# Performance work log

Measured on AMD Instinct MI355X. Metric: run time of the kernel, lower is better.

Reference implementation:

```python
import jax, jax.numpy as jnp
import numpy as np

D = 1024      # d_model
H = 16        # n_heads
M = 64        # n_memories
DK = D // H   # head dim
EPS = 1e-5    # LayerNorm eps


def setup_inputs() -> dict:
    key = jax.random.key(0)
    ks = jax.random.split(key, 16)
    B, N = 4, 1024
    s = 0.02
    return {
        "queries": jax.random.normal(ks[0], (B, N, D), jnp.float32),
        "keys": jax.random.normal(ks[1], (B, N, D), jnp.float32),
        "values": jax.random.normal(ks[2], (B, N, D), jnp.float32),
        "attention_mask": jax.random.randint(ks[3], (B, 1, 1, N), 0, 2, dtype=jnp.int32),
        "Wq": jax.random.normal(ks[4], (D, D), jnp.float32) * s,
        "bq": jnp.zeros((D,), jnp.float32),
        "Wk": jax.random.normal(ks[5], (D, D), jnp.float32) * s,
        "bk": jnp.zeros((D,), jnp.float32),
        "Wv": jax.random.normal(ks[6], (D, D), jnp.float32) * s,
        "bv": jnp.zeros((D,), jnp.float32),
        "Wo": jax.random.normal(ks[7], (D, D), jnp.float32) * s,
        "bo": jnp.zeros((D,), jnp.float32),
        "m_k": jax.random.normal(ks[8], (1, M, D), jnp.float32) * 0.01,
        "m_v": jax.random.normal(ks[9], (1, M, D), jnp.float32) * 0.01,
        "gamma": jnp.ones((D,), jnp.float32),
        "beta": jnp.zeros((D,), jnp.float32),
    }


def _layer_norm(x, gamma, beta):
    mu = jnp.mean(x, axis=-1, keepdims=True)
    var = jnp.var(x, axis=-1, keepdims=True)
    return (x - mu) * jax.lax.rsqrt(var + EPS) * gamma + beta


def reference(queries, keys, values, attention_mask,
              Wq, bq, Wk, bk, Wv, bv, Wo, bo, m_k, m_v, gamma, beta):
    B, Nq, _ = queries.shape
    Nk = keys.shape[1]
    scale = 1.0 / np.sqrt(DK)

    # projections (torch Linear: x @ W.T + b)
    q = (queries @ Wq.T + bq).reshape(B, Nq, H, DK).transpose(0, 2, 1, 3)  # b h nq d

    # memory-augmented K/V (memory tokens scaled as in the source)
    k_full = jnp.concatenate(
        [keys @ Wk.T + bk, jnp.broadcast_to(m_k * np.sqrt(DK), (B, M, D))], axis=1)
    v_full = jnp.concatenate(
        [values @ Wv.T + bv, jnp.broadcast_to(m_v * np.sqrt(M), (B, M, D))], axis=1)
    k = k_full.reshape(B, Nk + M, H, DK).transpose(0, 2, 1, 3)  # b h nk+m d
    v = v_full.reshape(B, Nk + M, H, DK).transpose(0, 2, 1, 3)  # b h nk+m d

    scores = jnp.einsum('bhqd,bhkd->bhqk', q, k) * scale  # [B,H,Nq,Nk+M]

    # partial masking: only the first Nk (non-memory) columns are maskable
    mask = jnp.concatenate(
        [attention_mask.astype(bool),
         jnp.zeros((B, 1, 1, M), dtype=bool)], axis=-1)
    scores = jnp.where(mask, -jnp.inf, scores)

    p_attn = jax.nn.softmax(scores, axis=-1)  # dropout p=0.0 -> identity
    out = jnp.einsum('bhqk,bhkd->bhqd', p_attn, v)
    out = out.transpose(0, 2, 1, 3).reshape(B, Nq, D)
    out = out @ Wo.T + bo

    # residual + LayerNorm (outer dropout is identity at p=0.0)
    return _layer_norm(queries + out, gamma, beta)
```

## Files before the change

### kernel.cpp

```cpp
#include <hip/hip_runtime.h>


typedef __bf16 bf16;
typedef __bf16 bf16x8 __attribute__((ext_vector_type(8)));
typedef __bf16 bf16x4 __attribute__((ext_vector_type(4)));
typedef float  f32x4  __attribute__((ext_vector_type(4)));

#define NSEQ 1024
#define NKV  1088
#define DMODEL 1024

struct CvtArgs { const float* s[7]; const float* mk; const float* mv; };

__global__ __launch_bounds__(256) void prep(CvtArgs c, bf16* __restrict__ dst,
                                            bf16* __restrict__ Kb,
                                            bf16* __restrict__ Vt)
{
    int blk = blockIdx.x;
    if (blk < 8192) {
        size_t e = ((size_t)blk * 256 + threadIdx.x) * 8;
        const float* s;
        if (e < ((size_t)3 << 22)) {
            s = c.s[e >> 22] + (e & 0x3FFFFF);
        } else {
            size_t wq = e - ((size_t)3 << 22);
            s = c.s[3 + (wq >> 20)] + (wq & 0xFFFFF);
        }
        f32x4 a = *(const f32x4*)s;
        f32x4 b = *(const f32x4*)(s + 4);
        bf16x8 o;
        for (int i = 0; i < 4; i++) { o[i] = (bf16)a[i]; o[4 + i] = (bf16)b[i]; }
        *(bf16x8*)&dst[e] = o;
    } else {
        int i = (blk - 8192) * 256 + threadIdx.x;
        int b = i >> 16, md = i & 65535;
        int m = md >> 10, dcol = md & 1023;
        Kb[(size_t)b * (NKV * DMODEL) + (size_t)(NSEQ + m) * DMODEL + dcol]
            = (bf16)(c.mk[md] * 8.0f);
        Vt[((size_t)b * 1024 + dcol) * NKV + NSEQ + m] = (bf16)(c.mv[md] * 8.0f);
    }
}

typedef __attribute__((address_space(1))) void gas_void;
typedef __attribute__((address_space(3))) void las_void;

__device__ __forceinline__ void gload16(const bf16* g, bf16* l)
{
    __builtin_amdgcn_global_load_lds((gas_void*)g, (las_void*)l, 16, 0, 0);
}

struct GemmArgsB {
    const bf16* A;
    const bf16* W;
    const float* bias;
    bf16* C;
    int osK;
    int vt;
};

__global__ __launch_bounds__(256, 3) void gemm128_lds(GemmArgsB g0, GemmArgsB g1,
                                                      GemmArgsB g2)
{
    const GemmArgsB g = (blockIdx.z == 0) ? g0 : (blockIdx.z == 1) ? g1 : g2;
    __shared__ bf16 As[128][32];
    __shared__ bf16 Bs[128][32];
    const int t = threadIdx.x;
    const int lane = t & 63, w = t >> 6;
    const int qi = lane & 15, qq = lane >> 4;
    const int wrow = (w >> 1) * 64, wcol = (w & 1) * 64;
    const int bm = blockIdx.y * 128, bn = blockIdx.x * 128;

    const int srow = w * 32 + (lane >> 2);
    const int scol = (lane & 3) * 8;
    const bf16* Ag = g.A + (size_t)(bm + srow) * DMODEL + scol;
    const bf16* Wg = g.W + (size_t)(bn + srow) * DMODEL + scol;
    bf16* Al = &As[w * 32][0];
    bf16* Bl = &Bs[w * 32][0];

    f32x4 acc[4][4] = {};

#define STAGE(kt)                                                             \
    do {                                                                      \
        gload16(Ag + (kt),                 Al);                               \
        gload16(Ag + (kt) + 16 * DMODEL,   Al + 16 * 32);                     \
        gload16(Wg + (kt),                 Bl);                               \
        gload16(Wg + (kt) + 16 * DMODEL,   Bl + 16 * 32);                    \
    } while (0)

    STAGE(0);
    for (int kt = 0; kt < DMODEL; kt += 32) {
        __syncthreads();
        bf16x8 a[4], b[4];
        for (int i = 0; i < 4; i++)
            a[i] = *(const bf16x8*)&As[wrow + i * 16 + qi][qq * 8];
        for (int j = 0; j < 4; j++)
            b[j] = *(const bf16x8*)&Bs[wcol + j * 16 + qi][qq * 8];
        __syncthreads();
        if (kt + 32 < DMODEL) STAGE(kt + 32);
        for (int i = 0; i < 4; i++)
            for (int j = 0; j < 4; j++)
                acc[i][j] = __builtin_amdgcn_mfma_f32_16x16x32_bf16(
                    a[i], b[j], acc[i][j], 0, 0, 0);
    }
#undef STAGE

    for (int i = 0; i < 4; i++)
        for (int j = 0; j < 4; j++) {
            int row0 = bm + wrow + i * 16 + qq * 4;
            int col  = bn + wcol + j * 16 + qi;
            float bcol = g.bias[col];
            if (g.vt) {
                bf16x4 v;
                for (int r = 0; r < 4; r++) v[r] = (bf16)(acc[i][j][r] + bcol);
                size_t off = ((size_t)((row0 >> 10) * 16 + (col >> 6)) * 64 + (col & 63))
                           * NKV + (row0 & 1023);
                *(bf16x4*)&g.C[off] = v;
            } else {
                for (int r = 0; r < 4; r++) {
                    int row = row0 + r;
                    size_t off = (size_t)(row >> 10) * g.osK
                               + (size_t)(row & 1023) * DMODEL + col;
                    g.C[off] = (bf16)(acc[i][j][r] + bcol);
                }
            }
        }
}

struct GemmArgs {
    const void* A;
    const float* W;
    const float* bias;
    bf16* C;
    int osK;
    int vt;
};

template<bool ABF>
__global__ __launch_bounds__(256, 2) void gemm128(GemmArgs g0, GemmArgs g1, GemmArgs g2)
{
    const GemmArgs g = (blockIdx.z == 0) ? g0 : (blockIdx.z == 1) ? g1 : g2;
    __shared__ bf16 As[128][44];
    __shared__ bf16 Bs[128][44];
    const int t = threadIdx.x;
    const int lane = t & 63, w = t >> 6;
    const int qi = lane & 15, qq = lane >> 4;
    const int wrow = (w >> 1) * 64, wcol = (w & 1) * 64;
    const int bm = blockIdx.y * 128, bn = blockIdx.x * 128;
    const int sr = t >> 1, sc = (t & 1) * 16;

    f32x4 acc[4][4] = {};

    f32x4 pa[4];
    bf16x8 pab[2];
    f32x4 pw[4];

    const float* Wp = g.W + (size_t)(bn + sr) * DMODEL + sc;
    const float* Af = (const float*)g.A + (size_t)(bm + sr) * DMODEL + sc;
    const bf16*  Ab = (const bf16*)g.A + (size_t)(bm + sr) * DMODEL + sc;

#define LOAD_TILES(kt)                                                        \
    do {                                                                      \
        if (ABF) {                                                            \
            pab[0] = *(const bf16x8*)(Ab + (kt));                             \
            pab[1] = *(const bf16x8*)(Ab + (kt) + 8);                         \
        } else {                                                              \
            pa[0] = *(const f32x4*)(Af + (kt));                               \
            pa[1] = *(const f32x4*)(Af + (kt) + 4);                           \
            pa[2] = *(const f32x4*)(Af + (kt) + 8);                           \
            pa[3] = *(const f32x4*)(Af + (kt) + 12);                          \
        }                                                                     \
        pw[0] = *(const f32x4*)(Wp + (kt));                                   \
        pw[1] = *(const f32x4*)(Wp + (kt) + 4);                               \
        pw[2] = *(const f32x4*)(Wp + (kt) + 8);                               \
        pw[3] = *(const f32x4*)(Wp + (kt) + 12);                              \
    } while (0)

#define STORE_TILES()                                                         \
    do {                                                                      \
        if (ABF) {                                                            \
            *(bf16x8*)&As[sr][sc]     = pab[0];                               \
            *(bf16x8*)&As[sr][sc + 8] = pab[1];                               \
        } else {                                                              \
            bf16x8 v0, v1;                                                    \
            for (int i = 0; i < 4; i++) {                                     \
                v0[i] = (bf16)pa[0][i]; v0[4 + i] = (bf16)pa[1][i];           \
                v1[i] = (bf16)pa[2][i]; v1[4 + i] = (bf16)pa[3][i];           \
            }                                                                 \
            *(bf16x8*)&As[sr][sc]     = v0;                                   \
            *(bf16x8*)&As[sr][sc + 8] = v1;                                   \
        }                                                                     \
        {                                                                     \
            bf16x8 u0, u1;                                                    \
            for (int i = 0; i < 4; i++) {                                     \
                u0[i] = (bf16)pw[0][i]; u0[4 + i] = (bf16)pw[1][i];           \
                u1[i] = (bf16)pw[2][i]; u1[4 + i] = (bf16)pw[3][i];           \
            }                                                                 \
            *(bf16x8*)&Bs[sr][sc]     = u0;                                   \
            *(bf16x8*)&Bs[sr][sc + 8] = u1;                                   \
        }                                                                     \
    } while (0)

    LOAD_TILES(0);
    STORE_TILES();
    __syncthreads();

    for (int kt = 0; kt < DMODEL; kt += 32) {
        const bool more = (kt + 32) < DMODEL;
        if (more) LOAD_TILES(kt + 32);
        bf16x8 a[4], b[4];
        for (int i = 0; i < 4; i++)
            a[i] = *(const bf16x8*)&As[wrow + i * 16 + qi][qq * 8];
        for (int j = 0; j < 4; j++)
            b[j] = *(const bf16x8*)&Bs[wcol + j * 16 + qi][qq * 8];
        for (int i = 0; i < 4; i++)
            for (int j = 0; j < 4; j++)
                acc[i][j] = __builtin_amdgcn_mfma_f32_16x16x32_bf16(a[i], b[j], acc[i][j], 0, 0, 0);
        if (more) {
            __syncthreads();
            STORE_TILES();
            __syncthreads();
        }
    }
#undef LOAD_TILES
#undef STORE_TILES

    for (int i = 0; i < 4; i++)
        for (int j = 0; j < 4; j++) {
            int row0 = bm + wrow + i * 16 + qq * 4;
            int col  = bn + wcol + j * 16 + qi;
            float bcol = g.bias[col];
            if (g.vt) {
                bf16x4 v;
                for (int r = 0; r < 4; r++) v[r] = (bf16)(acc[i][j][r] + bcol);
                size_t off = ((size_t)((row0 >> 10) * 16 + (col >> 6)) * 64 + (col & 63))
                           * NKV + (row0 & 1023);
                *(bf16x4*)&g.C[off] = v;
            } else {
                for (int r = 0; r < 4; r++) {
                    int row = row0 + r;
                    size_t off = (size_t)(row >> 10) * g.osK
                               + (size_t)(row & 1023) * DMODEL + col;
                    g.C[off] = (bf16)(acc[i][j][r] + bcol);
                }
            }
        }
}

__global__ void fill_mem(const float* __restrict__ mk, const float* __restrict__ mv,
                         bf16* __restrict__ K, bf16* __restrict__ Vt)
{
    int i = blockIdx.x * 256 + threadIdx.x;
    int b = i >> 16, md = i & 65535;
    int m = md >> 10, dcol = md & 1023;
    K[(size_t)b * (NKV * DMODEL) + (size_t)(NSEQ + m) * DMODEL + dcol]
        = (bf16)(mk[md] * 8.0f);
    Vt[((size_t)b * 1024 + dcol) * NKV + NSEQ + m] = (bf16)(mv[md] * 8.0f);
}

__global__ __launch_bounds__(256) void attn_flash(const bf16* Q,
        const bf16* __restrict__ K, const bf16* __restrict__ Vt,
        const int* __restrict__ mask, bf16* O)
{
    __shared__ bf16  sK[64][72];
    __shared__ bf16  sV[64][72];
    __shared__ bf16  sP[4][16][72];
    __shared__ __align__(16) float sM[NKV];
    const int t = threadIdx.x, lane = t & 63, w = t >> 6;
    int bh, q0;
    if (gridDim.y == 64) {
        int lin = blockIdx.y * 16 + blockIdx.x;
        bh = ((lin & 7) << 3) | ((lin >> 3) & 7);
        q0 = (lin >> 6) * 64;
    } else {
        bh = blockIdx.y;
        q0 = blockIdx.x * 64;
    }
    const int b = bh >> 4, h = bh & 15;
    const int sr = t >> 2, sc = (t & 3) * 16;
    const int qi = lane & 15, qq = lane >> 4;

    for (int j = t; j < NKV; j += 256)
        sM[j] = (j < NSEQ && mask[b * NSEQ + j] != 0) ? -3.0e38f : 0.0f;

    const size_t qbase = (size_t)(b * NSEQ + q0 + w * 16 + qi) * DMODEL
                       + h * 64 + qq * 8;
    bf16x8 qa0 = *(const bf16x8*)&Q[qbase];
    bf16x8 qa1 = *(const bf16x8*)&Q[qbase + 32];
    for (int i = 0; i < 8; i++) {
        qa0[i] = (bf16)((float)qa0[i] * 0.125f);
        qa1[i] = (bf16)((float)qa1[i] * 0.125f);
    }

    const bf16* kbase = K + (size_t)(b * NKV + sr) * DMODEL + h * 64 + sc;
    const bf16* vbase = Vt + ((size_t)bh * 64 + sr) * NKV + sc;

    bf16x8 pk0, pk1, pv0, pv1;
#define LOAD_KV(jt)                                                           \
    do {                                                                      \
        const bf16* kp = kbase + (size_t)(jt) * 64 * DMODEL;                  \
        pk0 = *(const bf16x8*)kp;                                             \
        pk1 = *(const bf16x8*)(kp + 8);                                       \
        const bf16* vp = vbase + (jt) * 64;                                   \
        pv0 = *(const bf16x8*)vp;                                             \
        pv1 = *(const bf16x8*)(vp + 8);                                       \
    } while (0)
#define STORE_KV()                                                            \
    do {                                                                      \
        *(bf16x8*)&sK[sr][sc]     = pk0;                                      \
        *(bf16x8*)&sK[sr][sc + 8] = pk1;                                      \
        *(bf16x8*)&sV[sr][sc]     = pv0;                                      \
        *(bf16x8*)&sV[sr][sc + 8] = pv1;                                      \
    } while (0)

    LOAD_KV(0);
    STORE_KV();

    float m_i0 = -3.0e38f, l_i0 = 0.f;
    f32x4 oacc[4] = {};

    for (int jt = 0; jt < 17; jt++) {
        const int j0 = jt * 64;
        __syncthreads();
        const bool more = jt < 16;
        if (more) LOAD_KV(jt + 1);

        f32x4 s[4];
        for (int g = 0; g < 4; g++) {
            bf16x8 k0 = *(const bf16x8*)&sK[g * 16 + qi][qq * 8];
            bf16x8 k1 = *(const bf16x8*)&sK[g * 16 + qi][32 + qq * 8];
            f32x4 a = *(const f32x4*)&sM[j0 + g * 16 + qq * 4];
            a = __builtin_amdgcn_mfma_f32_16x16x32_bf16(k0, qa0, a, 0, 0, 0);
            a = __builtin_amdgcn_mfma_f32_16x16x32_bf16(k1, qa1, a, 0, 0, 0);
            s[g] = a;
        }
        float rm = s[0][0];
        for (int g = 0; g < 4; g++)
            for (int r = 0; r < 4; r++) rm = fmaxf(rm, s[g][r]);
        rm = fmaxf(rm, __shfl_xor(rm, 16, 64));
        rm = fmaxf(rm, __shfl_xor(rm, 32, 64));
        float mnew = fmaxf(m_i0, rm);
        float alpha = __expf(m_i0 - mnew);
        m_i0 = mnew;
        float rs = 0.f;
        for (int g = 0; g < 4; g++)
            for (int r = 0; r < 4; r++) {
                float p = __expf(s[g][r] - mnew);
                s[g][r] = p;
                rs += p;
            }
        rs += __shfl_xor(rs, 16, 64);
        rs += __shfl_xor(rs, 32, 64);
        l_i0 = l_i0 * alpha + rs;

        for (int g = 0; g < 4; g++) {
            bf16x4 p4;
            for (int r = 0; r < 4; r++) p4[r] = (bf16)s[g][r];
            *(bf16x4*)&sP[w][qi][g * 16 + qq * 4] = p4;
        }
        float apv[4];
        for (int r = 0; r < 4; r++) apv[r] = __shfl(alpha, qq * 4 + r, 64);
        for (int g = 0; g < 4; g++)
            for (int r = 0; r < 4; r++) oacc[g][r] *= apv[r];

        bf16x8 af0 = *(const bf16x8*)&sP[w][qi][qq * 8];
        bf16x8 af1 = *(const bf16x8*)&sP[w][qi][32 + qq * 8];
        for (int g = 0; g < 4; g++) {
            bf16x8 v0 = *(const bf16x8*)&sV[g * 16 + qi][qq * 8];
            bf16x8 v1 = *(const bf16x8*)&sV[g * 16 + qi][32 + qq * 8];
            oacc[g] = __builtin_amdgcn_mfma_f32_16x16x32_bf16(af0, v0, oacc[g], 0, 0, 0);
            oacc[g] = __builtin_amdgcn_mfma_f32_16x16x32_bf16(af1, v1, oacc[g], 0, 0, 0);
        }
        __syncthreads();
        if (more) STORE_KV();
    }
#undef LOAD_KV
#undef STORE_KV

    float linv = 1.0f / l_i0;
    float inv[4];
    for (int r = 0; r < 4; r++) inv[r] = __shfl(linv, qq * 4 + r, 64);
    for (int g = 0; g < 4; g++)
        for (int r = 0; r < 4; r++) {
            int row = q0 + w * 16 + qq * 4 + r;
            int col = h * 64 + g * 16 + qi;
            O[(size_t)(b * NSEQ + row) * DMODEL + col] = (bf16)(oacc[g][r] * inv[r]);
        }
}

__global__ __launch_bounds__(256) void residual_ln(const float* __restrict__ X,
        const bf16* __restrict__ Y, const float* __restrict__ gamma,
        const float* __restrict__ beta, float* __restrict__ out)
{
    __shared__ float red[8];
    int row = blockIdx.x, t = threadIdx.x;
    size_t base = (size_t)row * DMODEL + t * 4;
    f32x4  xv = *(const f32x4*)&X[base];
    bf16x4 yv = *(const bf16x4*)&Y[base];
    float s[4], sum = 0.f, sq = 0.f;
    for (int i = 0; i < 4; i++) {
        s[i] = xv[i] + (float)yv[i];
        sum += s[i]; sq += s[i] * s[i];
    }
    for (int o = 32; o; o >>= 1) { sum += __shfl_xor(sum, o, 64); sq += __shfl_xor(sq, o, 64); }
    if ((t & 63) == 0) { red[t >> 6] = sum; red[4 + (t >> 6)] = sq; }
    __syncthreads();
    sum = red[0] + red[1] + red[2] + red[3];
    sq  = red[4] + red[5] + red[6] + red[7];
    float mean = sum * (1.0f / DMODEL);
    float var  = sq  * (1.0f / DMODEL) - mean * mean;
    float rstd = rsqrtf(var + 1e-5f);
    f32x4 gv = *(const f32x4*)&gamma[t * 4];
    f32x4 bv = *(const f32x4*)&beta[t * 4];
    f32x4 ov;
    for (int i = 0; i < 4; i++)
        ov[i] = (s[i] - mean) * rstd * gv[i] + bv[i];
    *(f32x4*)&out[base] = ov;
}

extern "C" void kernel_launch(void* const* d_in, const int* in_sizes, int n_in,
                              void* d_out, int out_size, void* d_ws, size_t ws_size,
                              hipStream_t stream)
{
    const float* queries = (const float*)d_in[0];
    const float* keys    = (const float*)d_in[1];
    const float* values  = (const float*)d_in[2];
    const int*   amask   = (const int*)d_in[3];
    const float* Wq = (const float*)d_in[4];  const float* bq = (const float*)d_in[5];
    const float* Wk = (const float*)d_in[6];  const float* bk = (const float*)d_in[7];
    const float* Wv = (const float*)d_in[8];  const float* bv = (const float*)d_in[9];
    const float* Wo = (const float*)d_in[10]; const float* bo = (const float*)d_in[11];
    const float* mk = (const float*)d_in[12]; const float* mv = (const float*)d_in[13];
    const float* gamma = (const float*)d_in[14]; const float* beta = (const float*)d_in[15];
    float* out = (float*)d_out;

    bf16* Qb = (bf16*)(out + (size_t)2 * 1024 * 1024);
    const size_t SB  = (size_t)NSEQ * DMODEL;
    const size_t KVB = (size_t)NKV * DMODEL;
    dim3 gb(256);

    const size_t need_r10 = (2 * 4 * KVB + 3 * 4 * SB + 4 * SB) * sizeof(bf16);

    if (ws_size >= need_r10) {
        bf16* Kb = (bf16*)d_ws;
        bf16* Vt = Kb + 4 * KVB;
        bf16* Ab = Vt + 4 * KVB;
        bf16* Wb = Ab + 12 * SB;
        bf16* PR = Ab;

        CvtArgs ca;
        ca.s[0] = queries; ca.s[1] = keys; ca.s[2] = values;
        ca.s[3] = Wq; ca.s[4] = Wk; ca.s[5] = Wv; ca.s[6] = Wo;
        ca.mk = mk; ca.mv = mv;
        prep<<<dim3(8192 + 1024), gb, 0, stream>>>(ca, Ab, Kb, Vt);

        GemmArgsB gq{Ab,           Wb,           bq, Qb, (int)SB,  0};
        GemmArgsB gk{Ab + 4 * SB,  Wb + SB,      bk, Kb, (int)KVB, 0};
        GemmArgsB gv{Ab + 8 * SB,  Wb + 2 * SB,  bv, Vt, 0,        1};
        gemm128_lds<<<dim3(8, 32, 3), gb, 0, stream>>>(gq, gk, gv);
        attn_flash<<<dim3(16, 64), gb, 0, stream>>>(Qb, Kb, Vt, amask, Qb);
        GemmArgsB go{Qb, Wb + 3 * SB, bo, PR, (int)SB, 0};
        gemm128_lds<<<dim3(8, 32, 1), gb, 0, stream>>>(go, go, go);
        residual_ln<<<dim3(4096), gb, 0, stream>>>(queries, PR, gamma, beta, out);
    } else if (ws_size >= (size_t)2 * 4 * KVB * sizeof(bf16)) {
        bf16* Kb = (bf16*)d_ws;
        bf16* Vt = Kb + 4 * KVB;
        bf16* PR = Kb;

        GemmArgs gq{queries, Wq, bq, Qb, (int)SB,  0};
        GemmArgs gk{keys,    Wk, bk, Kb, (int)KVB, 0};
        GemmArgs gv{values,  Wv, bv, Vt, 0,        1};
        gemm128<false><<<dim3(8, 32, 3), gb, 0, stream>>>(gq, gk, gv);
        fill_mem<<<dim3(1024), gb, 0, stream>>>(mk, mv, Kb, Vt);
        attn_flash<<<dim3(16, 64), gb, 0, stream>>>(Qb, Kb, Vt, amask, Qb);
        GemmArgs go{Qb, Wo, bo, PR, (int)SB, 0};
        gemm128<true><<<dim3(8, 32, 1), gb, 0, stream>>>(go, go, go);
        residual_ln<<<dim3(4096), gb, 0, stream>>>(queries, PR, gamma, beta, out);
    } else {
        bf16* Kb = (bf16*)d_ws;
        bf16* Vt = Kb + KVB;
        bf16* PR = Kb;

        GemmArgs gq{queries, Wq, bq, Qb, (int)SB, 0};
        gemm128<false><<<dim3(8, 32, 1), gb, 0, stream>>>(gq, gq, gq);
        for (int b = 0; b < 4; b++) {
            GemmArgs gk{keys   + b * SB, Wk, bk, Kb, 0, 0};
            GemmArgs gv{values + b * SB, Wv, bv, Vt, 0, 1};
            gemm128<false><<<dim3(8, 8, 2), gb, 0, stream>>>(gk, gv, gv);
            fill_mem<<<dim3(256), gb, 0, stream>>>(mk, mv, Kb, Vt);
            attn_flash<<<dim3(16, 16), gb, 0, stream>>>(Qb + b * SB, Kb, Vt,
                                                        amask + b * NSEQ, Qb + b * SB);
            GemmArgs go{Qb + b * SB, Wo, bo, PR, 0, 0};
            gemm128<true><<<dim3(8, 8, 1), gb, 0, stream>>>(go, go, go);
            residual_ln<<<dim3(1024), gb, 0, stream>>>(queries + b * SB, PR,
                                                       gamma, beta, out + b * SB);
        }
    }
}
```

Measured before the change: 243.3 us.

## Rework flash attention to 32x32 MFMA with 128-row query tiles

```diff
diff --git a/kernel.cpp b/kernel.cpp
--- a/kernel.cpp
+++ b/kernel.cpp
@@ -4,7 +4,10 @@
 typedef __bf16 bf16;
 typedef __bf16 bf16x8 __attribute__((ext_vector_type(8)));
 typedef __bf16 bf16x4 __attribute__((ext_vector_type(4)));
+typedef __bf16 bf16x2 __attribute__((ext_vector_type(2)));
 typedef float  f32x4  __attribute__((ext_vector_type(4)));
+typedef float  f32x16 __attribute__((ext_vector_type(16)));
+typedef unsigned uintx4 __attribute__((ext_vector_type(4)));
 
 #define NSEQ 1024
 #define NKV  1088
@@ -257,38 +260,42 @@
     Vt[((size_t)b * 1024 + dcol) * NKV + NSEQ + m] = (bf16)(mv[md] * 8.0f);
 }
 
+__device__ __forceinline__ unsigned pkbf(float a, float b)
+{
+    bf16x2 t; t[0] = (bf16)a; t[1] = (bf16)b;
+    unsigned u; __builtin_memcpy(&u, &t, 4); return u;
+}
+
 __global__ __launch_bounds__(256) void attn_flash(const bf16* Q,
         const bf16* __restrict__ K, const bf16* __restrict__ Vt,
         const int* __restrict__ mask, bf16* O)
 {
-    __shared__ bf16  sK[64][72];
-    __shared__ bf16  sV[64][72];
-    __shared__ bf16  sP[4][16][72];
+    __shared__ bf16 sKV[2][64][72];
     __shared__ __align__(16) float sM[NKV];
     const int t = threadIdx.x, lane = t & 63, w = t >> 6;
     int bh, q0;
     if (gridDim.y == 64) {
-        int lin = blockIdx.y * 16 + blockIdx.x;
+        int lin = blockIdx.y * gridDim.x + blockIdx.x;
         bh = ((lin & 7) << 3) | ((lin >> 3) & 7);
-        q0 = (lin >> 6) * 64;
+        q0 = (lin >> 6) * 128;
     } else {
         bh = blockIdx.y;
-        q0 = blockIdx.x * 64;
+        q0 = blockIdx.x * 128;
     }
     const int b = bh >> 4, h = bh & 15;
     const int sr = t >> 2, sc = (t & 3) * 16;
-    const int qi = lane & 15, qq = lane >> 4;
+    const int lq = lane & 31, hi = lane >> 5;
 
     for (int j = t; j < NKV; j += 256)
         sM[j] = (j < NSEQ && mask[b * NSEQ + j] != 0) ? -3.0e38f : 0.0f;
 
-    const size_t qbase = (size_t)(b * NSEQ + q0 + w * 16 + qi) * DMODEL
-                       + h * 64 + qq * 8;
-    bf16x8 qa0 = *(const bf16x8*)&Q[qbase];
-    bf16x8 qa1 = *(const bf16x8*)&Q[qbase + 32];
-    for (int i = 0; i < 8; i++) {
-        qa0[i] = (bf16)((float)qa0[i] * 0.125f);
-        qa1[i] = (bf16)((float)qa1[i] * 0.125f);
+    const size_t qrow = (size_t)(b * NSEQ + q0 + w * 32 + lq) * DMODEL + h * 64;
+    bf16x8 qf[4];
+#pragma unroll
+    for (int c = 0; c < 4; c++) {
+        bf16x8 v = *(const bf16x8*)&Q[qrow + c * 16 + hi * 8];
+        for (int i = 0; i < 8; i++) v[i] = (bf16)((float)v[i] * 0.125f);
+        qf[c] = v;
     }
 
     const bf16* kbase = K + (size_t)(b * NKV + sr) * DMODEL + h * 64 + sc;
@@ -306,17 +313,17 @@
     } while (0)
 #define STORE_KV()                                                            \
     do {                                                                      \
-        *(bf16x8*)&sK[sr][sc]     = pk0;                                      \
-        *(bf16x8*)&sK[sr][sc + 8] = pk1;                                      \
-        *(bf16x8*)&sV[sr][sc]     = pv0;                                      \
-        *(bf16x8*)&sV[sr][sc + 8] = pv1;                                      \
+        *(bf16x8*)&sKV[0][sr][sc]     = pk0;                                  \
+        *(bf16x8*)&sKV[0][sr][sc + 8] = pk1;                                  \
+        *(bf16x8*)&sKV[1][sr][sc]     = pv0;                                  \
+        *(bf16x8*)&sKV[1][sr][sc + 8] = pv1;                                  \
     } while (0)
 
     LOAD_KV(0);
     STORE_KV();
 
-    float m_i0 = -3.0e38f, l_i0 = 0.f;
-    f32x4 oacc[4] = {};
+    float m_i = -3.0e38f, l_i = 0.f;
+    f32x16 oacc0 = {}, oacc1 = {};
 
     for (int jt = 0; jt < 17; jt++) {
         const int j0 = jt * 64;
@@ -324,51 +331,78 @@
         const bool more = jt < 16;
         if (more) LOAD_KV(jt + 1);
 
-        f32x4 s[4];
-        for (int g = 0; g < 4; g++) {
-            bf16x8 k0 = *(const bf16x8*)&sK[g * 16 + qi][qq * 8];
-            bf16x8 k1 = *(const bf16x8*)&sK[g * 16 + qi][32 + qq * 8];
-            f32x4 a = *(const f32x4*)&sM[j0 + g * 16 + qq * 4];
-            a = __builtin_amdgcn_mfma_f32_16x16x32_bf16(k0, qa0, a, 0, 0, 0);
-            a = __builtin_amdgcn_mfma_f32_16x16x32_bf16(k1, qa1, a, 0, 0, 0);
-            s[g] = a;
-        }
-        float rm = s[0][0];
-        for (int g = 0; g < 4; g++)
-            for (int r = 0; r < 4; r++) rm = fmaxf(rm, s[g][r]);
-        rm = fmaxf(rm, __shfl_xor(rm, 16, 64));
+        f32x16 accs[2];
+#pragma unroll
+        for (int kb = 0; kb < 2; kb++) {
+#pragma unroll
+            for (int g2 = 0; g2 < 4; g2++) {
+                f32x4 m4 = *(const f32x4*)&sM[j0 + kb * 32 + 8 * g2 + 4 * hi];
+                accs[kb][4 * g2 + 0] = m4[0];
+                accs[kb][4 * g2 + 1] = m4[1];
+                accs[kb][4 * g2 + 2] = m4[2];
+                accs[kb][4 * g2 + 3] = m4[3];
+            }
+#pragma unroll
+            for (int c = 0; c < 4; c++) {
+                bf16x8 kf = *(const bf16x8*)&sKV[0][kb * 32 + lq][c * 16 + hi * 8];
+                accs[kb] = __builtin_amdgcn_mfma_f32_32x32x16_bf16(
+                    kf, qf[c], accs[kb], 0, 0, 0);
+            }
+        }
+
+        float rm = accs[0][0];
+#pragma unroll
+        for (int r = 1; r < 16; r++) rm = fmaxf(rm, accs[0][r]);
+#pragma unroll
+        for (int r = 0; r < 16; r++) rm = fmaxf(rm, accs[1][r]);
         rm = fmaxf(rm, __shfl_xor(rm, 32, 64));
-        float mnew = fmaxf(m_i0, rm);
-        float alpha = __expf(m_i0 - mnew);
-        m_i0 = mnew;
+        float mnew = fmaxf(m_i, rm);
+        float alpha = __expf(m_i - mnew);
+        m_i = mnew;
         float rs = 0.f;
-        for (int g = 0; g < 4; g++)
-            for (int r = 0; r < 4; r++) {
-                float p = __expf(s[g][r] - mnew);
-                s[g][r] = p;
+#pragma unroll
+        for (int kb = 0; kb < 2; kb++)
+#pragma unroll
+            for (int r = 0; r < 16; r++) {
+                float p = __expf(accs[kb][r] - mnew);
+                accs[kb][r] = p;
                 rs += p;
             }
-        rs += __shfl_xor(rs, 16, 64);
         rs += __shfl_xor(rs, 32, 64);
-        l_i0 = l_i0 * alpha + rs;
-
-        for (int g = 0; g < 4; g++) {
-            bf16x4 p4;
-            for (int r = 0; r < 4; r++) p4[r] = (bf16)s[g][r];
-            *(bf16x4*)&sP[w][qi][g * 16 + qq * 4] = p4;
-        }
-        float apv[4];
-        for (int r = 0; r < 4; r++) apv[r] = __shfl(alpha, qq * 4 + r, 64);
-        for (int g = 0; g < 4; g++)
-            for (int r = 0; r < 4; r++) oacc[g][r] *= apv[r];
-
-        bf16x8 af0 = *(const bf16x8*)&sP[w][qi][qq * 8];
-        bf16x8 af1 = *(const bf16x8*)&sP[w][qi][32 + qq * 8];
-        for (int g = 0; g < 4; g++) {
-            bf16x8 v0 = *(const bf16x8*)&sV[g * 16 + qi][qq * 8];
-            bf16x8 v1 = *(const bf16x8*)&sV[g * 16 + qi][32 + qq * 8];
-            oacc[g] = __builtin_amdgcn_mfma_f32_16x16x32_bf16(af0, v0, oacc[g], 0, 0, 0);
-            oacc[g] = __builtin_amdgcn_mfma_f32_16x16x32_bf16(af1, v1, oacc[g], 0, 0, 0);
+        l_i = l_i * alpha + rs;
+
+        unsigned dwv[16];
+#pragma unroll
+        for (int kb = 0; kb < 2; kb++)
+#pragma unroll
+            for (int a = 0; a < 4; a++) {
+                dwv[kb * 8 + 2 * a]     = pkbf(accs[kb][4 * a], accs[kb][4 * a + 1]);
+                dwv[kb * 8 + 2 * a + 1] = pkbf(accs[kb][4 * a + 2], accs[kb][4 * a + 3]);
+            }
+        bf16x8 pb[4];
+#pragma unroll
+        for (int i = 0; i < 4; i++) {
+            const int kb = i >> 1, ae = 2 * (i & 1), ao = ae + 1;
+            unsigned se0 = dwv[kb * 8 + 2 * ae], se1 = dwv[kb * 8 + 2 * ae + 1];
+            unsigned so0 = dwv[kb * 8 + 2 * ao], so1 = dwv[kb * 8 + 2 * ao + 1];
+            unsigned s0 = hi ? se0 : so0, s1 = hi ? se1 : so1;
+            unsigned k0 = hi ? so0 : se0, k1 = hi ? so1 : se1;
+            unsigned r0 = __shfl_xor((int)s0, 32, 64);
+            unsigned r1 = __shfl_xor((int)s1, 32, 64);
+            uintx4 cw;
+            cw[0] = hi ? r0 : k0; cw[1] = hi ? r1 : k1;
+            cw[2] = hi ? k0 : r0; cw[3] = hi ? k1 : r1;
+            __builtin_memcpy(&pb[i], &cw, 16);
+        }
+
+#pragma unroll
+        for (int r = 0; r < 16; r++) { oacc0[r] *= alpha; oacc1[r] *= alpha; }
+#pragma unroll
+        for (int c = 0; c < 4; c++) {
+            bf16x8 vf0 = *(const bf16x8*)&sKV[1][lq][c * 16 + hi * 8];
+            bf16x8 vf1 = *(const bf16x8*)&sKV[1][32 + lq][c * 16 + hi * 8];
+            oacc0 = __builtin_amdgcn_mfma_f32_32x32x16_bf16(vf0, pb[c], oacc0, 0, 0, 0);
+            oacc1 = __builtin_amdgcn_mfma_f32_32x32x16_bf16(vf1, pb[c], oacc1, 0, 0, 0);
         }
         __syncthreads();
         if (more) STORE_KV();
@@ -376,15 +410,23 @@
 #undef LOAD_KV
 #undef STORE_KV
 
-    float linv = 1.0f / l_i0;
-    float inv[4];
-    for (int r = 0; r < 4; r++) inv[r] = __shfl(linv, qq * 4 + r, 64);
-    for (int g = 0; g < 4; g++)
-        for (int r = 0; r < 4; r++) {
-            int row = q0 + w * 16 + qq * 4 + r;
-            int col = h * 64 + g * 16 + qi;
-            O[(size_t)(b * NSEQ + row) * DMODEL + col] = (bf16)(oacc[g][r] * inv[r]);
-        }
+    float linv = 1.0f / l_i;
+    __syncthreads();
+    bf16 (*sO)[72] = reinterpret_cast<bf16(*)[72]>(&sKV[0][0][0]);
+#pragma unroll
+    for (int r = 0; r < 16; r++) {
+        int dl = (r & 3) + 8 * (r >> 2) + 4 * hi;
+        sO[w * 32 + lq][dl]      = (bf16)(oacc0[r] * linv);
+        sO[w * 32 + lq][32 + dl] = (bf16)(oacc1[r] * linv);
+    }
+    __syncthreads();
+    {
+        int row = t >> 1, ch = (t & 1) * 32;
+        bf16* dst = &O[(size_t)(b * NSEQ + q0 + row) * DMODEL + h * 64 + ch];
+#pragma unroll
+        for (int k = 0; k < 4; k++)
+            *(bf16x8*)(dst + k * 8) = *(const bf16x8*)&sO[row][ch + k * 8];
+    }
 }
 
 __global__ __launch_bounds__(256) void residual_ln(const float* __restrict__ X,
@@ -457,7 +499,7 @@
         GemmArgsB gk{Ab + 4 * SB,  Wb + SB,      bk, Kb, (int)KVB, 0};
         GemmArgsB gv{Ab + 8 * SB,  Wb + 2 * SB,  bv, Vt, 0,        1};
         gemm128_lds<<<dim3(8, 32, 3), gb, 0, stream>>>(gq, gk, gv);
-        attn_flash<<<dim3(16, 64), gb, 0, stream>>>(Qb, Kb, Vt, amask, Qb);
+        attn_flash<<<dim3(8, 64), gb, 0, stream>>>(Qb, Kb, Vt, amask, Qb);
         GemmArgsB go{Qb, Wb + 3 * SB, bo, PR, (int)SB, 0};
         gemm128_lds<<<dim3(8, 32, 1), gb, 0, stream>>>(go, go, go);
         residual_ln<<<dim3(4096), gb, 0, stream>>>(queries, PR, gamma, beta, out);
@@ -471,7 +513,7 @@
         GemmArgs gv{values,  Wv, bv, Vt, 0,        1};
         gemm128<false><<<dim3(8, 32, 3), gb, 0, stream>>>(gq, gk, gv);
         fill_mem<<<dim3(1024), gb, 0, stream>>>(mk, mv, Kb, Vt);
-        attn_flash<<<dim3(16, 64), gb, 0, stream>>>(Qb, Kb, Vt, amask, Qb);
+        attn_flash<<<dim3(8, 64), gb, 0, stream>>>(Qb, Kb, Vt, amask, Qb);
         GemmArgs go{Qb, Wo, bo, PR, (int)SB, 0};
         gemm128<true><<<dim3(8, 32, 1), gb, 0, stream>>>(go, go, go);
         residual_ln<<<dim3(4096), gb, 0, stream>>>(queries, PR, gamma, beta, out);
@@ -487,8 +529,8 @@
             GemmArgs gv{values + b * SB, Wv, bv, Vt, 0, 1};
             gemm128<false><<<dim3(8, 8, 2), gb, 0, stream>>>(gk, gv, gv);
             fill_mem<<<dim3(256), gb, 0, stream>>>(mk, mv, Kb, Vt);
-            attn_flash<<<dim3(16, 16), gb, 0, stream>>>(Qb + b * SB, Kb, Vt,
-                                                        amask + b * NSEQ, Qb + b * SB);
+            attn_flash<<<dim3(8, 16), gb, 0, stream>>>(Qb + b * SB, Kb, Vt,
+                                                       amask + b * NSEQ, Qb + b * SB);
             GemmArgs go{Qb + b * SB, Wo, bo, PR, 0, 0};
             gemm128<true><<<dim3(8, 8, 1), gb, 0, stream>>>(go, go, go);
             residual_ln<<<dim3(1024), gb, 0, stream>>>(queries + b * SB, PR,
```

Result: faster. 236.4 us (-2.9%).
